# Performance work log

Measured on AMD Instinct MI355X. Metric: run time of the kernel, lower is better.

The kernel has to match this reference:

```python
import jax, jax.numpy as jnp
import numpy as np

N_NODES = 100000
N_EDGES = 1600000
IN_FEATS, HID_FEATS, OUT_FEATS = 64, 64, 32


def setup_inputs() -> dict:
    key = jax.random.key(0)
    ks = jax.random.split(key, 8)
    x = jax.random.normal(ks[0], (N_NODES, IN_FEATS), dtype=jnp.float32)
    edge_index = jax.random.randint(ks[1], (2, N_EDGES), 0, N_NODES, dtype=jnp.int64)
    s1 = 1.0 / np.sqrt(IN_FEATS)
    s2 = 1.0 / np.sqrt(HID_FEATS)
    return {
        "x": x,
        "edge_index": edge_index,
        "W1l": jax.random.uniform(ks[2], (IN_FEATS, HID_FEATS), jnp.float32, -s1, s1),
        "W1r": jax.random.uniform(ks[3], (IN_FEATS, HID_FEATS), jnp.float32, -s1, s1),
        "b1": jnp.zeros((HID_FEATS,), jnp.float32),
        "W2l": jax.random.uniform(ks[4], (HID_FEATS, OUT_FEATS), jnp.float32, -s2, s2),
        "W2r": jax.random.uniform(ks[5], (HID_FEATS, OUT_FEATS), jnp.float32, -s2, s2),
        "b2": jnp.zeros((OUT_FEATS,), jnp.float32),
    }


def _mean_aggregate(h, src, dst, n_nodes):
    # gather source features, scatter-mean into destination nodes
    msg_sum = jax.ops.segment_sum(h[src], dst, num_segments=n_nodes)  # [N, D]
    cnt = jax.ops.segment_sum(jnp.ones(src.shape, h.dtype), dst, num_segments=n_nodes)
    return msg_sum / jnp.maximum(cnt, 1.0)[:, None]  # zero in-degree -> 0


def _sage_conv(h, src, dst, Wl, Wr, b):
    # PyG SAGEConv: lin_l(mean_j x_j) + lin_r(x_i); bias lives in lin_l
    agg = _mean_aggregate(h, src, dst, h.shape[0])
    return agg @ Wl + h @ Wr + b


def reference(x, edge_index, W1l, W1r, b1, W2l, W2r, b2):
    src, dst = edge_index[0], edge_index[1]
    h = jax.nn.relu(_sage_conv(x, src, dst, W1l, W1r, b1))
    out = _sage_conv(h, src, dst, W2l, W2r, b2)
    return out
```

## Files before the change

kernel.cpp:

```cpp
#include <hip/hip_runtime.h>

#define NN 100000
#define NE 1600000
#define NBK 392
#define CAPB 6144
#define CVTB 6250

typedef __attribute__((ext_vector_type(8))) short bf16x8;
typedef __attribute__((ext_vector_type(4))) float f32x4;

__device__ __forceinline__ unsigned short f2b(float f) {
  unsigned b = __float_as_uint(f);
  unsigned r = b + 0x7FFF + ((b >> 16) & 1);
  return (unsigned short)(r >> 16);
}

__global__ void k_zero(int* __restrict__ g) {
  if (threadIdx.x < NBK) g[threadIdx.x] = 0;
}

__global__ void k_pre(const float* __restrict__ x, unsigned short* __restrict__ xb,
                      const float* __restrict__ W1l, const float* __restrict__ W1r,
                      unsigned short* __restrict__ WT1,
                      const float* __restrict__ W2l, const float* __restrict__ W2r,
                      unsigned short* __restrict__ WT2,
                      const int* __restrict__ src, const int* __restrict__ dst,
                      int* __restrict__ gcur, unsigned* __restrict__ pairbuf) {
  __shared__ int hist[NBK];
  __shared__ int sc[512];
  __shared__ int base[NBK], lofs[NBK];
  __shared__ unsigned epk[4096];
  __shared__ unsigned short ebk[4096];
  int t = threadIdx.x;
  int b = blockIdx.x;
  if (b < CVTB) {
    int i = (b * 256 + t) * 4;
    float4 v = *(const float4*)(x + i);
    ushort4 o;
    o.x = f2b(v.x); o.y = f2b(v.y); o.z = f2b(v.z); o.w = f2b(v.w);
    *(ushort4*)(xb + i) = o;
    return;
  }
  if (b == CVTB) {
    for (int i = t; i < 64 * 128; i += 256) {
      int f = i >> 7, k = i & 127;
      WT1[i] = f2b((k < 64) ? W1l[k * 64 + f] : W1r[(k - 64) * 64 + f]);
    }
    return;
  }
  if (b == CVTB + 1) {
    for (int i = t; i < 32 * 128; i += 256) {
      int f = i >> 7, k = i & 127;
      WT2[i] = f2b((k < 64) ? W2l[k * 32 + f] : W2r[(k - 64) * 32 + f]);
    }
    return;
  }
  int pb = b - (CVTB + 2);
  for (int i = t; i < NBK; i += 256) { hist[i] = 0; lofs[i] = 0; }
  __syncthreads();
  unsigned pk[16]; int bk[16];
  int e0 = pb * 4096 + t;
#pragma unroll
  for (int j = 0; j < 16; ++j) {
    int e = e0 + j * 256;
    if (e < NE) {
      int d = dst[e], s = src[e];
      bk[j] = d >> 8;
      pk[j] = ((unsigned)s << 8) | (unsigned)(d & 255);
      atomicAdd(&hist[bk[j]], 1);
    } else bk[j] = -1;
  }
  __syncthreads();
  sc[t] = (t < NBK) ? hist[t] : 0;
  sc[t + 256] = (t + 256 < NBK) ? hist[t + 256] : 0;
  __syncthreads();
  for (int off = 1; off < 512; off <<= 1) {
    int v0 = (t >= off) ? sc[t - off] : 0;
    int v1 = sc[t + 256 - off];
    __syncthreads();
    sc[t] += v0;
    sc[t + 256] += v1;
    __syncthreads();
  }
  for (int i = t; i < NBK; i += 256) {
    int h = hist[i];
    base[i] = atomicAdd(&gcur[i], h);
    hist[i] = sc[i] - h;
  }
  __syncthreads();
#pragma unroll
  for (int j = 0; j < 16; ++j) {
    if (bk[j] >= 0) {
      int pos = hist[bk[j]] + atomicAdd(&lofs[bk[j]], 1);
      epk[pos] = pk[j];
      ebk[pos] = (unsigned short)bk[j];
    }
  }
  __syncthreads();
  int cb = sc[511];
  for (int i = t; i < cb; i += 256) {
    unsigned p = epk[i];
    int bb = ebk[i];
    int slot = base[bb] + (i - hist[bb]);
    if (slot < CAPB) pairbuf[(size_t)bb * CAPB + slot] = p;
  }
}

__global__ void k_partB(const unsigned* __restrict__ pairbuf, const int* __restrict__ gcur,
                        int* __restrict__ esrc, uint2* __restrict__ rowp2) {
  __shared__ int cnt[256], cur[256], ssum[256];
  __shared__ int ebuf[CAPB];
  int b = blockIdx.x, t = threadIdx.x;
  int cb = gcur[b]; if (cb > CAPB) cb = CAPB;
  cnt[t] = 0;
  __syncthreads();
  const unsigned* pb = pairbuf + (size_t)b * CAPB;
  for (int i = t; i < cb; i += 256) atomicAdd(&cnt[pb[i] & 255], 1);
  __syncthreads();
  int a0 = cnt[t];
  ssum[t] = a0;
  __syncthreads();
  for (int off = 1; off < 256; off <<= 1) {
    int tmp = (t >= off) ? ssum[t - off] : 0;
    __syncthreads();
    ssum[t] += tmp;
    __syncthreads();
  }
  int ex = ssum[t] - a0;
  cur[t] = ex;
  __syncthreads();
  int n = b * 256 + t;
  if (n < NN) rowp2[n] = make_uint2((unsigned)(b * CAPB + ex),
                                    (unsigned)(b * CAPB + ex + a0));
  for (int i = t; i < cb; i += 256) {
    unsigned p = pb[i];
    int pos = atomicAdd(&cur[p & 255], 1);
    ebuf[pos] = (int)(p >> 8);
  }
  __syncthreads();
  for (int i = t; i < cb; i += 256) esrc[(size_t)b * CAPB + i] = ebuf[i];
}

__global__ void k_agg(const uint2* __restrict__ fb64, const uint2* __restrict__ rowp2,
                      const int* __restrict__ esrc, uint2* __restrict__ aggb64) {
  int tid = blockIdx.x * 256 + threadIdx.x;
  int node = tid >> 4;
  int c16 = tid & 15;
  int qbase = (threadIdx.x & 63) & 48;
  uint2 rp = rowp2[node];
  int beg = (int)rp.x, deg = (int)(rp.y - rp.x);
  float a0 = 0.f, a1 = 0.f, a2 = 0.f, a3 = 0.f;

  for (int r0 = 0; r0 < deg; r0 += 16) {
    int rem = deg - r0; if (rem > 16) rem = 16;
    int idxv = esrc[beg + r0 + (c16 < rem ? c16 : 0)];
    int sv[16];
#pragma unroll
    for (int j = 0; j < 16; ++j) sv[j] = __shfl(idxv, qbase + j);
    uint2 v[16];
#pragma unroll
    for (int j = 0; j < 16; ++j)
      if (j < rem) v[j] = fb64[(size_t)sv[j] * 16 + c16];
    __builtin_amdgcn_sched_barrier(0);
#pragma unroll
    for (int j = 0; j < 16; ++j)
      if (j < rem) {
        a0 += __uint_as_float(v[j].x << 16);
        a1 += __uint_as_float(v[j].x & 0xFFFF0000u);
        a2 += __uint_as_float(v[j].y << 16);
        a3 += __uint_as_float(v[j].y & 0xFFFF0000u);
      }
  }
  float inv = (deg > 0) ? (1.0f / (float)deg) : 0.f;
  uint2 o;
  o.x = (unsigned)f2b(a0 * inv) | ((unsigned)f2b(a1 * inv) << 16);
  o.y = (unsigned)f2b(a2 * inv) | ((unsigned)f2b(a3 * inv) << 16);
  aggb64[(size_t)node * 16 + c16] = o;
}

template <int NF>
__global__ __launch_bounds__(256) void k_gemm(
    const unsigned short* __restrict__ aggb, const unsigned short* __restrict__ featb,
    const unsigned short* __restrict__ WT, const float* __restrict__ bias,
    float* __restrict__ out, unsigned short* __restrict__ ob, int relu) {
  __shared__ unsigned short As[64 * 128];
  __shared__ unsigned short Ws[NF * 128];
  int tid = threadIdx.x;
  int n0 = blockIdx.x * 64;
  int lane = tid & 63, wr = tid >> 6;

  for (int cch = tid; cch < 64 * 16; cch += 256) {
    int r = cch >> 4, s = cch & 15;
    int n = n0 + r;
    bf16x8 v = {0, 0, 0, 0, 0, 0, 0, 0};
    if (n < NN) {
      const unsigned short* p = (s < 8) ? (aggb + (size_t)n * 64 + s * 8)
                                        : (featb + (size_t)n * 64 + (s - 8) * 8);
      v = *(const bf16x8*)p;
    }
    *(bf16x8*)(&As[r * 128 + ((s ^ (r & 15)) << 3)]) = v;
  }
  for (int cch = tid; cch < NF * 16; cch += 256) {
    int f = cch >> 4, s = cch & 15;
    bf16x8 v = *(const bf16x8*)(WT + f * 128 + s * 8);
    *(bf16x8*)(&Ws[f * 128 + ((s ^ (f & 15)) << 3)]) = v;
  }
  __syncthreads();

  int l15 = lane & 15, lg = lane >> 4;
  int arow = wr * 16 + l15;
  f32x4 acc[NF / 16];
#pragma unroll
  for (int ct = 0; ct < NF / 16; ++ct) acc[ct] = (f32x4){0.f, 0.f, 0.f, 0.f};

#pragma unroll
  for (int k0 = 0; k0 < 4; ++k0) {
    int sa = k0 * 4 + lg;
    bf16x8 a = *(const bf16x8*)(&As[arow * 128 + ((sa ^ (arow & 15)) << 3)]);
#pragma unroll
    for (int ct = 0; ct < NF / 16; ++ct) {
      int bcol = ct * 16 + l15;
      bf16x8 b = *(const bf16x8*)(&Ws[bcol * 128 + ((sa ^ (bcol & 15)) << 3)]);
      acc[ct] = __builtin_amdgcn_mfma_f32_16x16x32_bf16(a, b, acc[ct], 0, 0, 0);
    }
  }

#pragma unroll
  for (int ct = 0; ct < NF / 16; ++ct) {
    int f = ct * 16 + l15;
    float bv = bias[f];
#pragma unroll
    for (int r = 0; r < 4; ++r) {
      int n = n0 + wr * 16 + lg * 4 + r;
      if (n >= NN) continue;
      float v = acc[ct][r] + bv;
      if (relu) v = fmaxf(v, 0.f);
      if (out) out[(size_t)n * NF + f] = v;
      if (ob) ob[(size_t)n * NF + f] = f2b(v);
    }
  }
}

extern "C" void kernel_launch(void* const* d_in, const int* in_sizes, int n_in,
                              void* d_out, int out_size, void* d_ws, size_t ws_size,
                              hipStream_t stream) {
  const float* x   = (const float*)d_in[0];
  const int*   ei  = (const int*)d_in[1];
  const float* W1l = (const float*)d_in[2];
  const float* W1r = (const float*)d_in[3];
  const float* b1  = (const float*)d_in[4];
  const float* W2l = (const float*)d_in[5];
  const float* W2r = (const float*)d_in[6];
  const float* b2  = (const float*)d_in[7];
  const int* src = ei;
  const int* dst = ei + NE;
  float* out = (float*)d_out;

  char* ws = (char*)d_ws;
  size_t off = 0;
  auto take = [&](size_t bytes) -> char* {
    char* p = ws + off;
    off = (off + bytes + 255) & ~(size_t)255;
    return p;
  };
  int*      gcur    = (int*)take((size_t)NBK * 4);
  unsigned* pairbuf = (unsigned*)take((size_t)NBK * CAPB * 4);
  int*      esrc    = (int*)take((size_t)NBK * CAPB * 4);
  uint2*    rowp2   = (uint2*)take((size_t)NN * 8);
  unsigned short* aggb = (unsigned short*)take((size_t)NN * 64 * 2);
  unsigned short* xb   = (unsigned short*)take((size_t)NN * 64 * 2);
  unsigned short* hb   = (unsigned short*)take((size_t)NN * 64 * 2);
  unsigned short* WT1  = (unsigned short*)take((size_t)64 * 128 * 2);
  unsigned short* WT2  = (unsigned short*)take((size_t)32 * 128 * 2);

  int nbA = (NE + 4095) / 4096;
  k_zero<<<1, 512, 0, stream>>>(gcur);
  k_pre<<<CVTB + 2 + nbA, 256, 0, stream>>>(x, xb, W1l, W1r, WT1, W2l, W2r, WT2,
                                            src, dst, gcur, pairbuf);
  k_partB<<<NBK, 256, 0, stream>>>(pairbuf, gcur, esrc, rowp2);

  int nbG = (NN + 63) / 64;
  k_agg<<<NN / 16, 256, 0, stream>>>((const uint2*)xb, rowp2, esrc, (uint2*)aggb);
  k_gemm<64><<<nbG, 256, 0, stream>>>(aggb, xb, WT1, b1, nullptr, hb, 1);
  k_agg<<<NN / 16, 256, 0, stream>>>((const uint2*)hb, rowp2, esrc, (uint2*)aggb);
  k_gemm<32><<<nbG, 256, 0, stream>>>(aggb, hb, WT2, b2, out, nullptr, 0);
}
```

Measured before the change: 131.1 us.

## Split preprocessing kernel, shrink partition chunks, widen bucket-sort blocks

Measured after the change: 133.8 us. +2.1%, slower.

```diff
diff --git a/kernel.cpp b/kernel.cpp
--- a/kernel.cpp
+++ b/kernel.cpp
@@ -5,6 +5,7 @@
 #define NBK 392
 #define CAPB 6144
 #define CVTB 6250
+#define EPA 2048
 
 typedef __attribute__((ext_vector_type(8))) short bf16x8;
 typedef __attribute__((ext_vector_type(4))) float f32x4;
@@ -15,22 +16,11 @@
   return (unsigned short)(r >> 16);
 }
 
-__global__ void k_zero(int* __restrict__ g) {
-  if (threadIdx.x < NBK) g[threadIdx.x] = 0;
-}
-
-__global__ void k_pre(const float* __restrict__ x, unsigned short* __restrict__ xb,
-                      const float* __restrict__ W1l, const float* __restrict__ W1r,
-                      unsigned short* __restrict__ WT1,
-                      const float* __restrict__ W2l, const float* __restrict__ W2r,
-                      unsigned short* __restrict__ WT2,
-                      const int* __restrict__ src, const int* __restrict__ dst,
-                      int* __restrict__ gcur, unsigned* __restrict__ pairbuf) {
-  __shared__ int hist[NBK];
-  __shared__ int sc[512];
-  __shared__ int base[NBK], lofs[NBK];
-  __shared__ unsigned epk[4096];
-  __shared__ unsigned short ebk[4096];
+__global__ void k_cvtpre(const float* __restrict__ x, unsigned short* __restrict__ xb,
+                         const float* __restrict__ W1l, const float* __restrict__ W1r,
+                         unsigned short* __restrict__ WT1,
+                         const float* __restrict__ W2l, const float* __restrict__ W2r,
+                         unsigned short* __restrict__ WT2, int* __restrict__ gcur) {
   int t = threadIdx.x;
   int b = blockIdx.x;
   if (b < CVTB) {
@@ -42,26 +32,34 @@
     return;
   }
   if (b == CVTB) {
+    for (int i = t; i < NBK; i += 256) gcur[i] = 0;
     for (int i = t; i < 64 * 128; i += 256) {
       int f = i >> 7, k = i & 127;
       WT1[i] = f2b((k < 64) ? W1l[k * 64 + f] : W1r[(k - 64) * 64 + f]);
     }
     return;
   }
-  if (b == CVTB + 1) {
-    for (int i = t; i < 32 * 128; i += 256) {
-      int f = i >> 7, k = i & 127;
-      WT2[i] = f2b((k < 64) ? W2l[k * 32 + f] : W2r[(k - 64) * 32 + f]);
-    }
-    return;
-  }
-  int pb = b - (CVTB + 2);
+  for (int i = t; i < 32 * 128; i += 256) {
+    int f = i >> 7, k = i & 127;
+    WT2[i] = f2b((k < 64) ? W2l[k * 32 + f] : W2r[(k - 64) * 32 + f]);
+  }
+}
+
+__global__ void k_partA(const int* __restrict__ src, const int* __restrict__ dst,
+                        int* __restrict__ gcur, unsigned* __restrict__ pairbuf) {
+  __shared__ int hist[NBK];
+  __shared__ int sc[512];
+  __shared__ int base[NBK], lofs[NBK];
+  __shared__ unsigned epk[EPA];
+  __shared__ unsigned short ebk[EPA];
+  int t = threadIdx.x;
+  int pb = blockIdx.x;
   for (int i = t; i < NBK; i += 256) { hist[i] = 0; lofs[i] = 0; }
   __syncthreads();
-  unsigned pk[16]; int bk[16];
-  int e0 = pb * 4096 + t;
-#pragma unroll
-  for (int j = 0; j < 16; ++j) {
+  unsigned pk[EPA / 256]; int bk[EPA / 256];
+  int e0 = pb * EPA + t;
+#pragma unroll
+  for (int j = 0; j < EPA / 256; ++j) {
     int e = e0 + j * 256;
     if (e < NE) {
       int d = dst[e], s = src[e];
@@ -89,7 +87,7 @@
   }
   __syncthreads();
 #pragma unroll
-  for (int j = 0; j < 16; ++j) {
+  for (int j = 0; j < EPA / 256; ++j) {
     if (bk[j] >= 0) {
       int pos = hist[bk[j]] + atomicAdd(&lofs[bk[j]], 1);
       epk[pos] = pk[j];
@@ -112,33 +110,35 @@
   __shared__ int ebuf[CAPB];
   int b = blockIdx.x, t = threadIdx.x;
   int cb = gcur[b]; if (cb > CAPB) cb = CAPB;
-  cnt[t] = 0;
+  if (t < 256) cnt[t] = 0;
   __syncthreads();
   const unsigned* pb = pairbuf + (size_t)b * CAPB;
-  for (int i = t; i < cb; i += 256) atomicAdd(&cnt[pb[i] & 255], 1);
-  __syncthreads();
-  int a0 = cnt[t];
-  ssum[t] = a0;
+  for (int i = t; i < cb; i += 512) atomicAdd(&cnt[pb[i] & 255], 1);
+  __syncthreads();
+  int a0 = (t < 256) ? cnt[t] : 0;
+  if (t < 256) ssum[t] = a0;
   __syncthreads();
   for (int off = 1; off < 256; off <<= 1) {
-    int tmp = (t >= off) ? ssum[t - off] : 0;
-    __syncthreads();
-    ssum[t] += tmp;
-    __syncthreads();
-  }
-  int ex = ssum[t] - a0;
-  cur[t] = ex;
-  __syncthreads();
-  int n = b * 256 + t;
-  if (n < NN) rowp2[n] = make_uint2((unsigned)(b * CAPB + ex),
-                                    (unsigned)(b * CAPB + ex + a0));
-  for (int i = t; i < cb; i += 256) {
+    int tmp = (t < 256 && t >= off) ? ssum[t - off] : 0;
+    __syncthreads();
+    if (t < 256) ssum[t] += tmp;
+    __syncthreads();
+  }
+  if (t < 256) {
+    int ex = ssum[t] - a0;
+    cur[t] = ex;
+    int n = b * 256 + t;
+    if (n < NN) rowp2[n] = make_uint2((unsigned)(b * CAPB + ex),
+                                      (unsigned)(b * CAPB + ex + a0));
+  }
+  __syncthreads();
+  for (int i = t; i < cb; i += 512) {
     unsigned p = pb[i];
     int pos = atomicAdd(&cur[p & 255], 1);
     ebuf[pos] = (int)(p >> 8);
   }
   __syncthreads();
-  for (int i = t; i < cb; i += 256) esrc[(size_t)b * CAPB + i] = ebuf[i];
+  for (int i = t; i < cb; i += 512) esrc[(size_t)b * CAPB + i] = ebuf[i];
 }
 
 __global__ void k_agg(const uint2* __restrict__ fb64, const uint2* __restrict__ rowp2,
@@ -273,11 +273,10 @@
   unsigned short* WT1  = (unsigned short*)take((size_t)64 * 128 * 2);
   unsigned short* WT2  = (unsigned short*)take((size_t)32 * 128 * 2);
 
-  int nbA = (NE + 4095) / 4096;
-  k_zero<<<1, 512, 0, stream>>>(gcur);
-  k_pre<<<CVTB + 2 + nbA, 256, 0, stream>>>(x, xb, W1l, W1r, WT1, W2l, W2r, WT2,
-                                            src, dst, gcur, pairbuf);
-  k_partB<<<NBK, 256, 0, stream>>>(pairbuf, gcur, esrc, rowp2);
+  int nbA = (NE + EPA - 1) / EPA;
+  k_cvtpre<<<CVTB + 2, 256, 0, stream>>>(x, xb, W1l, W1r, WT1, W2l, W2r, WT2, gcur);
+  k_partA<<<nbA, 256, 0, stream>>>(src, dst, gcur, pairbuf);
+  k_partB<<<NBK, 512, 0, stream>>>(pairbuf, gcur, esrc, rowp2);
 
   int nbG = (NN + 63) / 64;
   k_agg<<<NN / 16, 256, 0, stream>>>((const uint2*)xb, rowp2, esrc, (uint2*)aggb);
```
